# Kernel tuning notes

Hardware: AMD Instinct MI355X
Metric: run time of the kernel (lower is better)

## Reference

```python
import jax, jax.numpy as jnp
import numpy as np
from jax import lax

B, C, D, H, W = 4, 384, 16, 16, 16
DSTATE, DCONV, EXPAND = 16, 4, 2
DIN = C * EXPAND            # 768
DTRANK = (C + 15) // 16     # 24
EPS = 1e-5


def setup_inputs() -> dict:
    ks = jax.random.split(jax.random.key(0), 12)
    g = lambda k, shape, s=0.02: jax.random.normal(k, shape, jnp.float32) * s
    return {
        "x": jax.random.normal(ks[0], (B, C, D, H, W), jnp.float32),
        "gsc_w1": g(ks[1], (C, C, 3, 3, 3)), "gsc_b1": jnp.zeros((C,), jnp.float32),
        "gsc_w2": g(ks[2], (C, C, 3, 3, 3)), "gsc_b2": jnp.zeros((C,), jnp.float32),
        "gsc_w3": g(ks[3], (C, C, 1, 1, 1)), "gsc_b3": jnp.zeros((C,), jnp.float32),
        "gsc_w4": g(ks[4], (C, C, 1, 1, 1)), "gsc_b4": jnp.zeros((C,), jnp.float32),
        "ln_g": jnp.ones((C,), jnp.float32), "ln_b": jnp.zeros((C,), jnp.float32),
        "in_proj_w": g(ks[5], (2 * DIN, C)),
        "conv1d_w": g(ks[6], (DIN, 1, DCONV), 0.1), "conv1d_b": jnp.zeros((DIN,), jnp.float32),
        "x_proj_w": g(ks[7], (DTRANK + 2 * DSTATE, DIN)),
        "dt_proj_w": g(ks[8], (DIN, DTRANK), 0.1), "dt_proj_b": jnp.full((DIN,), -4.0, jnp.float32),
        "A_log": jnp.log(jnp.tile(jnp.arange(1, DSTATE + 1, dtype=jnp.float32), (DIN, 1))),
        "D_skip": jnp.ones((DIN,), jnp.float32),
        "out_proj_w": g(ks[9], (C, DIN)),
    }


def _conv3d(x, w, b, pad):
    y = lax.conv_general_dilated(x, w, (1, 1, 1), [(pad, pad)] * 3,
                                 dimension_numbers=("NCDHW", "OIDHW", "NCDHW"))
    return y + b[None, :, None, None, None]


def _inorm(x):  # InstanceNorm3d, affine=False, biased variance
    m = x.mean((2, 3, 4), keepdims=True)
    v = x.var((2, 3, 4), keepdims=True)
    return (x - m) * lax.rsqrt(v + EPS)


def _forward(x, gsc_w1, gsc_b1, gsc_w2, gsc_b2, gsc_w3, gsc_b3, gsc_w4, gsc_b4,
             ln_g, ln_b, in_proj_w, conv1d_w, conv1d_b, x_proj_w,
             dt_proj_w, dt_proj_b, A_log, D_skip, out_proj_w):
    relu = jax.nn.relu
    # ---- GSC block (residual gated spatial conv) ----
    x1 = relu(_inorm(_conv3d(x, gsc_w1, gsc_b1, 1)))
    x1 = relu(_inorm(_conv3d(x1, gsc_w2, gsc_b2, 1)))
    x2 = relu(_inorm(_conv3d(x, gsc_w3, gsc_b3, 0)))
    xg = relu(_inorm(_conv3d(x1 + x2, gsc_w4, gsc_b4, 0))) + x
    # ---- MambaLayer: flatten voxels to tokens ----
    Bn = xg.shape[0]
    L = D * H * W
    t = xg.reshape(Bn, C, L).swapaxes(1, 2)                     # [B, L, C]
    mu = t.mean(-1, keepdims=True)
    var = t.var(-1, keepdims=True)
    tn = (t - mu) * lax.rsqrt(var + EPS) * ln_g + ln_b          # LayerNorm
    # ---- Mamba block ----
    xz = tn @ in_proj_w.T                                       # [B, L, 2*DIN]
    xin, z = jnp.split(xz, 2, axis=-1)
    xc = xin.swapaxes(1, 2)                                     # [B, DIN, L]
    xc = lax.conv_general_dilated(xc, conv1d_w, (1,), [(DCONV - 1, 0)],
                                  dimension_numbers=("NCH", "OIH", "NCH"),
                                  feature_group_count=DIN)      # causal depthwise conv
    u = jax.nn.silu(xc + conv1d_b[None, :, None]).swapaxes(1, 2)  # [B, L, DIN]
    dbl = u @ x_proj_w.T                                        # [B, L, DTRANK+2N]
    dt, Bm, Cm = jnp.split(dbl, [DTRANK, DTRANK + DSTATE], axis=-1)
    dt = jax.nn.softplus(dt @ dt_proj_w.T + dt_proj_b)          # [B, L, DIN]
    A = -jnp.exp(A_log)                                         # [DIN, N]

    def step(h, inp):  # h: [B, DIN, N]
        dt_t, B_t, C_t, u_t = inp
        dA = jnp.exp(dt_t[:, :, None] * A)
        h = dA * h + (dt_t * u_t)[:, :, None] * B_t[:, None, :]
        return h, jnp.einsum("bdn,bn->bd", h, C_t)

    h0 = jnp.zeros((Bn, DIN, DSTATE), x.dtype)
    _, ys = lax.scan(step, h0, (dt.swapaxes(0, 1), Bm.swapaxes(0, 1),
                                Cm.swapaxes(0, 1), u.swapaxes(0, 1)))
    y = ys.swapaxes(0, 1) + u * D_skip                          # [B, L, DIN]
    y = y * jax.nn.silu(z)
    out = y @ out_proj_w.T                                      # [B, L, C]
    return out.swapaxes(1, 2).reshape(Bn, C, D, H, W)


def reference(x, gsc_w1, gsc_b1, gsc_w2, gsc_b2, gsc_w3, gsc_b3, gsc_w4, gsc_b4,
              ln_g, ln_b, in_proj_w, conv1d_w, conv1d_b, x_proj_w,
              dt_proj_w, dt_proj_b, A_log, D_skip, out_proj_w):
    return _forward(x, gsc_w1, gsc_b1, gsc_w2, gsc_b2, gsc_w3, gsc_b3, gsc_w4, gsc_b4,
                    ln_g, ln_b, in_proj_w, conv1d_w, conv1d_b, x_proj_w,
                    dt_proj_w, dt_proj_b, A_log, D_skip, out_proj_w)
```

## Files before the change

### kernel.cpp

```cpp
#include <hip/hip_runtime.h>
#include <math.h>

#define CDIM 384
#define SDIM 4096
#define BDIM 4
#define DINC 768
#define NST  16
#define NCHUNK 64
#define LCHUNK 64
#define PSTRIDE 6291456

typedef unsigned short ushort_t;
typedef unsigned int uint_t;
typedef __attribute__((ext_vector_type(4))) float f32x4;
typedef __attribute__((ext_vector_type(8))) short bf16x8;

__device__ __forceinline__ ushort_t f2bf(float f) {
    union { float f; uint_t u; } v; v.f = f;
    uint_t r = v.u + 0x7FFFu + ((v.u >> 16) & 1u);
    return (ushort_t)(r >> 16);
}
__device__ __forceinline__ float bf2f(ushort_t u) {
    union { uint_t i; float f; } v; v.i = ((uint_t)u) << 16; return v.f;
}
__device__ __forceinline__ uint_t pk2(float a, float b) {
    return (uint_t)f2bf(a) | ((uint_t)f2bf(b) << 16);
}
__device__ __forceinline__ void gl16(const ushort_t* g, ushort_t* l) {
    __builtin_amdgcn_global_load_lds(
        (const __attribute__((address_space(1))) void*)(g),
        (__attribute__((address_space(3))) void*)(l), 16, 0, 0);
}

__device__ __forceinline__ void wconv_body(const float* __restrict__ W,
                                           ushort_t* __restrict__ Wb, int idx) {
    const float* wp = W + (size_t)idx * 27;
#pragma unroll
    for (int tap = 0; tap < 27; ++tap)
        Wb[(size_t)tap * (CDIM * CDIM) + idx] = f2bf(wp[tap]);
}
__device__ __forceinline__ void cvt_body(const float* __restrict__ src,
                                         ushort_t* __restrict__ dst, int i) {
    float4 v = ((const float4*)src)[i];
    uint2 o; o.x = pk2(v.x, v.y); o.y = pk2(v.z, v.w);
    ((uint2*)dst)[i] = o;
}
__global__ __launch_bounds__(256)
void prep_weights_kernel(const float* w1, const float* w2, const float* w3,
                         const float* w4, const float* ipw, const float* opw,
                         const float* xpw,
                         ushort_t* Wb1, ushort_t* Wb2, ushort_t* w3b, ushort_t* w4b,
                         ushort_t* ipwb, ushort_t* opwb, ushort_t* xpwb) {
    const int bid = blockIdx.x, t = threadIdx.x;
    if      (bid < 576)  wconv_body(w1, Wb1, bid * 256 + t);
    else if (bid < 1152) wconv_body(w2, Wb2, (bid - 576) * 256 + t);
    else if (bid < 1296) cvt_body(w3, w3b, (bid - 1152) * 256 + t);
    else if (bid < 1440) cvt_body(w4, w4b, (bid - 1296) * 256 + t);
    else if (bid < 2016) cvt_body(ipw, ipwb, (bid - 1440) * 256 + t);
    else if (bid < 2304) cvt_body(opw, opwb, (bid - 2016) * 256 + t);
    else                 cvt_body(xpw, xpwb, (bid - 2304) * 256 + t);
}

__global__ __launch_bounds__(384)
void pad_kernel(const float* __restrict__ src, ushort_t* __restrict__ Xp) {
    const int blk = blockIdx.x;
    const int b = blk >> 8, d = (blk >> 4) & 15, h = blk & 15;
    const int ci = threadIdx.x;
    const float* sp = src + (size_t)(b * CDIM + ci) * SDIM + d * 256 + h * 16;
    ushort_t* dp = Xp + ((((size_t)(b * 18 + d + 1) * 18) + (h + 1)) * 18 + 1) * CDIM + ci;
#pragma unroll
    for (int w = 0; w < 16; ++w)
        dp[(size_t)w * CDIM] = f2bf(sp[w]);
}

__global__ __launch_bounds__(384)
void pad_fuse2_kernel(const float* __restrict__ P0, const float* __restrict__ P1,
                      const float* __restrict__ stats, ushort_t* __restrict__ Xp) {
    const int blk = blockIdx.x;
    const int b = blk >> 8, d = (blk >> 4) & 15, h = blk & 15;
    const int ci = threadIdx.x;
    const size_t o = (size_t)(b * CDIM + ci) * SDIM + d * 256 + h * 16;
    const float m = stats[(b * CDIM + ci) * 2], r = stats[(b * CDIM + ci) * 2 + 1];
    ushort_t* dp = Xp + ((((size_t)(b * 18 + d + 1) * 18) + (h + 1)) * 18 + 1) * CDIM + ci;
#pragma unroll
    for (int w = 0; w < 16; ++w) {
        const float v = P0[o + w] + P1[o + w];
        dp[(size_t)w * CDIM] = f2bf(fmaxf((v - m) * r, 0.f));
    }
}

__global__ __launch_bounds__(384)
void pad_fuse3_kernel(const float* __restrict__ P0, const float* __restrict__ P1,
                      const float* __restrict__ st2, const float* __restrict__ C3,
                      const float* __restrict__ st3, ushort_t* __restrict__ Xp) {
    const int blk = blockIdx.x;
    const int b = blk >> 8, d = (blk >> 4) & 15, h = blk & 15;
    const int ci = threadIdx.x;
    const size_t o = (size_t)(b * CDIM + ci) * SDIM + d * 256 + h * 16;
    const float m2 = st2[(b * CDIM + ci) * 2], r2 = st2[(b * CDIM + ci) * 2 + 1];
    const float m3 = st3[(b * CDIM + ci) * 2], r3 = st3[(b * CDIM + ci) * 2 + 1];
    ushort_t* dp = Xp + ((((size_t)(b * 18 + d + 1) * 18) + (h + 1)) * 18 + 1) * CDIM + ci;
#pragma unroll
    for (int w = 0; w < 16; ++w) {
        const float x1 = fmaxf((P0[o + w] + P1[o + w] - m2) * r2, 0.f);
        const float x2 = fmaxf((C3[o + w] - m3) * r3, 0.f);
        dp[(size_t)w * CDIM] = f2bf(x1 + x2);
    }
}

template<int MODE>
__global__ __launch_bounds__(256)
void conv_kernel(const ushort_t* __restrict__ Xp, const ushort_t* __restrict__ Wb,
                 const ushort_t* __restrict__ W3, float* __restrict__ Y01,
                 float* __restrict__ Y2) {
    const int wid = blockIdx.x;
    const int ntid = wid & 127;
    const int rest = wid >> 7;
    const int co0 = (rest % 3) * 128;
    const int zz  = rest / 3;
    const int b  = ntid >> 5;
    const int d  = (ntid >> 1) & 15;
    const int h0 = (ntid & 1) * 8;
    const int t = threadIdx.x;
    const int lane = t & 63;
    const int wv = t >> 6;
    const int wy = wv >> 1, wx = wv & 1;

    const bool is1x1 = (MODE == 2) || (MODE == 1 && zz == 2);
    const ushort_t* Wsrc; int tap0, iters, kd0, kh0, kw0; float* Y;
    if (is1x1) {
        Wsrc = W3; tap0 = 0; iters = 12; kd0 = 1; kh0 = 1; kw0 = 1; Y = Y2;
    } else {
        Wsrc = Wb; tap0 = zz ? 14 : 0; iters = (zz ? 13 : 14) * 12;
        kd0 = zz ? 1 : 0; kh0 = zz ? 1 : 0; kw0 = zz ? 2 : 0;
        Y = Y01 + (size_t)zz * PSTRIDE;
    }

    __shared__ __align__(16) ushort_t As[4096];
    __shared__ __align__(16) ushort_t Bs[4096];

    f32x4 acc[4][4];
#pragma unroll
    for (int i = 0; i < 4; ++i)
#pragma unroll
        for (int j = 0; j < 4; ++j) acc[i][j] = (f32x4){0.f, 0.f, 0.f, 0.f};

    const int l4 = lane >> 2;
    const int cg = (((lane & 3) ^ ((lane >> 3) & 3)) << 3);
    int aTC[2], bTC[2];
#pragma unroll
    for (int i = 0; i < 2; ++i) {
        const int r = wv * 32 + i * 16 + l4;
        aTC[i] = (co0 + r) * CDIM + cg;
        bTC[i] = ((r >> 4) * 18 + (r & 15)) * CDIM + cg;
    }
    ushort_t* lA[2] = { &As[wv * 1024], &As[wv * 1024 + 512] };
    ushort_t* lB[2] = { &Bs[wv * 1024], &Bs[wv * 1024 + 512] };

    int aoff = tap0 * (CDIM * CDIM);
    int goff = (((b * 18 + d + kd0) * 18 + (h0 + kh0)) * 18 + kw0) * CDIM;
    int c12 = 0, ckw = kw0, ckh = kh0;

    const int lm = lane & 15;
    const int sw8 = (((lane >> 4) ^ ((lm >> 1) & 3)) << 3);
    const int rA0 = (wy * 64 + lm) * 32 + sw8;
    const int rB0 = (wx * 64 + lm) * 32 + sw8;

    for (int idx = 0; idx < iters; ++idx) {
#pragma unroll
        for (int i = 0; i < 2; ++i) {
            gl16(Wsrc + aoff + aTC[i], lA[i]);
            gl16(Xp + goff + bTC[i], lB[i]);
        }
        aoff += 32; goff += 32;
        if (++c12 == 12) {
            c12 = 0;
            aoff += CDIM * CDIM - CDIM;
            if (++ckw == 3) {
                ckw = 0;
                if (++ckh == 3) { ckh = 0; goff += 109440; }
                else goff += 5760;
            }
        }
        __syncthreads();
        bf16x8 af[4], bfr[4];
#pragma unroll
        for (int mi = 0; mi < 4; ++mi)
            af[mi] = *reinterpret_cast<const bf16x8*>(&As[rA0 + mi * 512]);
#pragma unroll
        for (int ni = 0; ni < 4; ++ni)
            bfr[ni] = *reinterpret_cast<const bf16x8*>(&Bs[rB0 + ni * 512]);
#pragma unroll
        for (int mi = 0; mi < 4; ++mi)
#pragma unroll
            for (int ni = 0; ni < 4; ++ni)
                acc[mi][ni] = __builtin_amdgcn_mfma_f32_16x16x32_bf16(
                    af[mi], bfr[ni], acc[mi][ni], 0, 0, 0);
        __syncthreads();
    }

    const int coB = co0 + wy * 64 + (lane >> 4) * 4;
    const int nB  = wx * 64 + lm;
#pragma unroll
    for (int mi = 0; mi < 4; ++mi) {
#pragma unroll
        for (int ni = 0; ni < 4; ++ni) {
            const int nl = nB + ni * 16;
            const int s = d * 256 + (h0 + (nl >> 4)) * 16 + (nl & 15);
            float* yp = Y + ((size_t)b * CDIM + (coB + mi * 16)) * SDIM + s;
#pragma unroll
            for (int j = 0; j < 4; ++j)
                yp[(size_t)j * SDIM] = acc[mi][ni][j];
        }
    }
}

template<int EPI>
__global__ __launch_bounds__(256)
void gemm_mfma_kernel(const ushort_t* __restrict__ A, const ushort_t* __restrict__ Bw,
                      void* __restrict__ Cv, void* __restrict__ C2v,
                      int M, int N, int K, int ldc, int nx) {
    const int wid = blockIdx.x;
    const int n0 = (wid % nx) * 128;
    const int m0 = (wid / nx) * 128;
    const int t = threadIdx.x;
    const int lane = t & 63;
    const int wy = (t >> 6) >> 1, wx = (t >> 6) & 1;

    __shared__ ushort_t As[2][128 * 40];
    __shared__ ushort_t Bs[2][128 * 40];

    f32x4 acc[4][4];
#pragma unroll
    for (int i = 0; i < 4; ++i)
#pragma unroll
        for (int j = 0; j < 4; ++j) acc[i][j] = (f32x4){0.f, 0.f, 0.f, 0.f};

    const int arow = t >> 1, half = t & 1;
    const int wA = arow * 40 + half * 16;
    const int lm = lane & 15, lk = (lane >> 4) * 8;
    const int rA0 = (wy * 64 + lm) * 40 + lk;
    const int rB0 = (wx * 64 + lm) * 40 + lk;

    uint4 ra0, ra1, rb0, rb1;

    auto loadg = [&](int kk) {
        const int kb = kk * 32 + half * 16;
        const uint4* pa = reinterpret_cast<const uint4*>(
            A + (size_t)(m0 + arow) * K + kb);
        ra0 = pa[0]; ra1 = pa[1];
        if (n0 + arow < N) {
            const uint4* pb = reinterpret_cast<const uint4*>(
                Bw + (size_t)(n0 + arow) * K + kb);
            rb0 = pb[0]; rb1 = pb[1];
        } else {
            rb0 = make_uint4(0, 0, 0, 0); rb1 = rb0;
        }
    };
    auto lwrite = [&](int buf) {
        *reinterpret_cast<uint4*>(&As[buf][wA])     = ra0;
        *reinterpret_cast<uint4*>(&As[buf][wA + 8]) = ra1;
        *reinterpret_cast<uint4*>(&Bs[buf][wA])     = rb0;
        *reinterpret_cast<uint4*>(&Bs[buf][wA + 8]) = rb1;
    };

    const int KI = K >> 5;
    loadg(0);
    lwrite(0);
    __syncthreads();

    int buf = 0;
    for (int kk = 0; kk < KI; ++kk) {
        const bool more = (kk + 1) < KI;
        if (more) loadg(kk + 1);
        bf16x8 af[4], bfr[4];
#pragma unroll
        for (int mi = 0; mi < 4; ++mi)
            af[mi] = *reinterpret_cast<const bf16x8*>(&As[buf][rA0 + mi * 640]);
#pragma unroll
        for (int ni = 0; ni < 4; ++ni)
            bfr[ni] = *reinterpret_cast<const bf16x8*>(&Bs[buf][rB0 + ni * 640]);
#pragma unroll
        for (int mi = 0; mi < 4; ++mi)
#pragma unroll
            for (int ni = 0; ni < 4; ++ni)
                acc[mi][ni] = __builtin_amdgcn_mfma_f32_16x16x32_bf16(
                    af[mi], bfr[ni], acc[mi][ni], 0, 0, 0);
        if (more) lwrite(buf ^ 1);
        __syncthreads();
        buf ^= 1;
    }

    const int mB = m0 + wy * 64 + (lane >> 4) * 4;
    const int nB = n0 + wx * 64 + lm;
#pragma unroll
    for (int mi = 0; mi < 4; ++mi) {
#pragma unroll
        for (int ni = 0; ni < 4; ++ni) {
            const int n = nB + ni * 16;
            if (EPI == 2) {
                const int mrow = mB + mi * 16;
                const int bb = mrow >> 12, l = mrow & 4095;
                float4 st = {acc[mi][ni][0], acc[mi][ni][1],
                             acc[mi][ni][2], acc[mi][ni][3]};
                *reinterpret_cast<float4*>(
                    (float*)Cv + ((size_t)(bb * CDIM + n)) * SDIM + l) = st;
            } else {
#pragma unroll
                for (int j = 0; j < 4; ++j) {
                    const int m = mB + mi * 16 + j;
                    const float v = acc[mi][ni][j];
                    if (EPI == 0) {
                        if (n < N) ((float*)Cv)[(size_t)m * ldc + n] = v;
                    } else {
                        if (n < DINC) ((ushort_t*)Cv)[(size_t)m * DINC + n] = f2bf(v);
                        else ((ushort_t*)C2v)[(size_t)m * DINC + (n - DINC)] = f2bf(v);
                    }
                }
            }
        }
    }
}

__device__ __forceinline__ void stats_reduce(float s, float ss, float* out) {
#pragma unroll
    for (int off = 32; off > 0; off >>= 1) {
        s += __shfl_down(s, off);
        ss += __shfl_down(ss, off);
    }
    __shared__ float rs[4], rss[4];
    const int wid = threadIdx.x >> 6;
    if ((threadIdx.x & 63) == 0) { rs[wid] = s; rss[wid] = ss; }
    __syncthreads();
    if (threadIdx.x == 0) {
        float S = rs[0] + rs[1] + rs[2] + rs[3];
        float SS = rss[0] + rss[1] + rss[2] + rss[3];
        float m = S * (1.f / SDIM);
        float var = SS * (1.f / SDIM) - m * m;
        out[0] = m;
        out[1] = rsqrtf(var + 1e-5f);
    }
}

__global__ __launch_bounds__(256)
void inorm_stats_combo_kernel(const float* __restrict__ P0, const float* __restrict__ P1,
                              float* __restrict__ SA, const float* __restrict__ X3,
                              float* __restrict__ SB) {
    const int bid = blockIdx.x;
    float s = 0.f, ss = 0.f;
    if (bid < 1536) {
        const float* p0 = P0 + (size_t)bid * SDIM;
        const float* p1 = P1 + (size_t)bid * SDIM;
        for (int i = threadIdx.x * 4; i < SDIM; i += 1024) {
            float4 a = *(const float4*)(p0 + i);
            float4 c = *(const float4*)(p1 + i);
            const float vx = a.x + c.x, vy = a.y + c.y, vz = a.z + c.z, vw = a.w + c.w;
            s += vx + vy + vz + vw;
            ss += vx * vx + vy * vy + vz * vz + vw * vw;
        }
        stats_reduce(s, ss, SA + bid * 2);
    } else {
        const int bc = bid - 1536;
        const float* xp = X3 + (size_t)bc * SDIM;
        for (int i = threadIdx.x * 4; i < SDIM; i += 1024) {
            float4 v = *(const float4*)(xp + i);
            s += v.x + v.y + v.z + v.w;
            ss += v.x * v.x + v.y * v.y + v.z * v.z + v.w * v.w;
        }
        stats_reduce(s, ss, SB + bc * 2);
    }
}

__global__ __launch_bounds__(256)
void inorm_stats_kernel(const float* __restrict__ X, float* __restrict__ stats) {
    const int bc = blockIdx.x;
    const float* xp = X + (size_t)bc * SDIM;
    float s = 0.f, ss = 0.f;
    for (int i = threadIdx.x * 4; i < SDIM; i += 1024) {
        float4 v = *(const float4*)(xp + i);
        s += v.x + v.y + v.z + v.w;
        ss += v.x * v.x + v.y * v.y + v.z * v.z + v.w * v.w;
    }
    stats_reduce(s, ss, stats + bc * 2);
}

__global__ __launch_bounds__(256)
void layernorm_kernel(const float* __restrict__ C4, const float* __restrict__ stats,
                      const float* __restrict__ X, const float* __restrict__ gam,
                      const float* __restrict__ bet, ushort_t* __restrict__ Tn) {
    const int token = blockIdx.x * 4 + (threadIdx.x >> 6);
    const int lane = threadIdx.x & 63;
    const int b = token >> 12, l = token & 4095;
    const size_t base = (size_t)b * CDIM * SDIM + l;
    float v[6];
    float s = 0.f, ss = 0.f;
#pragma unroll
    for (int i = 0; i < 6; ++i) {
        const int c = lane + i * 64;
        const size_t o = base + (size_t)c * SDIM;
        const float m = stats[(b * CDIM + c) * 2], r = stats[(b * CDIM + c) * 2 + 1];
        v[i] = fmaxf((C4[o] - m) * r, 0.f) + X[o];
        s += v[i]; ss += v[i] * v[i];
    }
#pragma unroll
    for (int off = 32; off > 0; off >>= 1) {
        s += __shfl_down(s, off);
        ss += __shfl_down(ss, off);
    }
    s = __shfl(s, 0); ss = __shfl(ss, 0);
    const float m = s * (1.f / CDIM);
    const float r = rsqrtf(ss * (1.f / CDIM) - m * m + 1e-5f);
    ushort_t* tp = Tn + (size_t)token * CDIM;
#pragma unroll
    for (int i = 0; i < 6; ++i) {
        const int c = lane + i * 64;
        tp[c] = f2bf((v[i] - m) * r * gam[c] + bet[c]);
    }
}

__global__ __launch_bounds__(256)
void gemm_dtproj_kernel(const float* __restrict__ A, const float* __restrict__ B,
                        ushort_t* __restrict__ C, const float* __restrict__ bias,
                        int M, int N, int K, int lda, int ldb, int ldc) {
    __shared__ __align__(16) float As[16][132];
    __shared__ __align__(16) float Bs[16][68];
    const int t = threadIdx.x;
    const int m0 = blockIdx.y * 128;
    const int n0 = blockIdx.x * 64;

    float acc[8][4];
#pragma unroll
    for (int i = 0; i < 8; ++i)
#pragma unroll
        for (int j = 0; j < 4; ++j) acc[i][j] = 0.f;

    const int mr = (t & 15) * 8;
    const int nr = (t >> 4) * 4;

    for (int k0 = 0; k0 < K; k0 += 16) {
#pragma unroll
        for (int idx = 0; idx < 8; ++idx) {
            const int e = idx * 256 + t;
            const int k = e & 15, m = e >> 4;
            float v = 0.f;
            if (k0 + k < K) v = A[(size_t)(m0 + m) * lda + (k0 + k)];
            As[k][m] = v;
        }
#pragma unroll
        for (int idx = 0; idx < 4; ++idx) {
            const int e = idx * 256 + t;
            const int k = e & 15, n = e >> 4;
            float v = 0.f;
            if ((n0 + n) < N && (k0 + k) < K) v = B[(size_t)(n0 + n) * ldb + (k0 + k)];
            Bs[k][n] = v;
        }
        __syncthreads();
#pragma unroll
        for (int k = 0; k < 16; ++k) {
            float4 a0 = *(const float4*)&As[k][mr];
            float4 a1 = *(const float4*)&As[k][mr + 4];
            float4 b0 = *(const float4*)&Bs[k][nr];
            const float av[8] = {a0.x, a0.y, a0.z, a0.w, a1.x, a1.y, a1.z, a1.w};
            const float bv[4] = {b0.x, b0.y, b0.z, b0.w};
#pragma unroll
            for (int i = 0; i < 8; ++i)
#pragma unroll
                for (int j = 0; j < 4; ++j)
                    acc[i][j] = fmaf(av[i], bv[j], acc[i][j]);
        }
        __syncthreads();
    }

#pragma unroll
    for (int i = 0; i < 8; ++i) {
        const int m = m0 + mr + i;
#pragma unroll
        for (int j = 0; j < 4; ++j) {
            const int n = n0 + nr + j;
            if (n >= N) continue;
            float v = acc[i][j] + bias[n];
            v = (v > 20.f) ? v : log1pf(__expf(v));
            C[(size_t)m * ldc + n] = f2bf(v);
        }
    }
}

__global__ __launch_bounds__(256)
void dwconv_silu_kernel(const ushort_t* __restrict__ Xin, const float* __restrict__ W,
                        const float* __restrict__ bias, ushort_t* __restrict__ U) {
    const int dch = blockIdx.x * 256 + threadIdx.x;
    const int l0 = blockIdx.y * 4, b = blockIdx.z;
    const float4 w4 = ((const float4*)W)[dch];
    const float wk[4] = {w4.x, w4.y, w4.z, w4.w};
    const float bs = bias[dch];
    const size_t base = ((size_t)b * 4096 + l0) * DINC + dch;
    float r[7];
#pragma unroll
    for (int k = 0; k < 7; ++k) {
        const int ll = l0 - 3 + k;
        r[k] = (ll >= 0) ? bf2f(Xin[base + (size_t)(k - 3) * DINC]) : 0.f;
    }
#pragma unroll
    for (int j = 0; j < 4; ++j) {
        float acc = bs;
#pragma unroll
        for (int k = 0; k < 4; ++k) acc = fmaf(r[j + k], wk[k], acc);
        U[base + (size_t)j * DINC] = f2bf(acc / (1.f + __expf(-acc)));
    }
}

__global__ __launch_bounds__(256)
void scan_phase1_kernel(const ushort_t* __restrict__ DT, const ushort_t* __restrict__ U,
                        const float* __restrict__ DBL, const float* __restrict__ A_log,
                        float* __restrict__ HOUT, float* __restrict__ SDT) {
    const int b = blockIdx.z, chunk = blockIdx.y;
    const int dch = blockIdx.x * 256 + threadIdx.x;
    float Arow[16];
#pragma unroll
    for (int n = 0; n < NST; ++n) Arow[n] = -__expf(A_log[dch * NST + n]);

    __shared__ float bcs[LCHUNK][16];
    const size_t tokbase = (size_t)b * 4096 + chunk * LCHUNK;
#pragma unroll
    for (int idx = 0; idx < 4; ++idx) {
        const int e = idx * 256 + threadIdx.x;
        bcs[e >> 4][e & 15] = DBL[(tokbase + (e >> 4)) * 56 + 24 + (e & 15)];
    }
    __syncthreads();

    size_t off = tokbase * DINC + dch;
    float h[16];
#pragma unroll
    for (int n = 0; n < NST; ++n) h[n] = 0.f;
    float sdt = 0.f;
    float cdt = bf2f(DT[off]), cu = bf2f(U[off]);
    for (int t = 0; t < LCHUNK; ++t) {
        float ndt = 0.f, nu = 0.f;
        if (t < LCHUNK - 1) { ndt = bf2f(DT[off + DINC]); nu = bf2f(U[off + DINC]); }
        sdt += cdt;
        const float du = cdt * cu;
#pragma unroll
        for (int n = 0; n < NST; ++n)
            h[n] = __expf(cdt * Arow[n]) * h[n] + du * bcs[t][n];
        off += DINC;
        cdt = ndt; cu = nu;
    }
    float* hp = HOUT + (((size_t)(b * DINC + dch) * NCHUNK + chunk) << 4);
#pragma unroll
    for (int n = 0; n < NST; ++n) hp[n] = h[n];
    SDT[(size_t)(b * DINC + dch) * NCHUNK + chunk] = sdt;
}

__global__ __launch_bounds__(256)
void scan_phase2_kernel(float* __restrict__ HOUT, const float* __restrict__ SDT,
                        const float* __restrict__ A_log) {
    const int t = blockIdx.x * 256 + threadIdx.x;
    const int b = t / (DINC * NST);
    const int rem = t - b * (DINC * NST);
    const int d = rem >> 4, n = rem & 15;
    const float An = -__expf(A_log[d * NST + n]);
    float* hp = HOUT + (((size_t)(b * DINC + d) * NCHUNK) << 4) + n;
    const float* sp = SDT + (size_t)(b * DINC + d) * NCHUNK;
    float H = 0.f;
    for (int c = 0; c < NCHUNK; ++c) {
        const float tmp = hp[c * 16];
        const float dA = __expf(An * sp[c]);
        hp[c * 16] = H;
        H = dA * H + tmp;
    }
}

__global__ __launch_bounds__(256)
void scan_phase3_kernel(ushort_t* __restrict__ DT, const ushort_t* __restrict__ U,
                        const float* __restrict__ DBL, const ushort_t* __restrict__ Z,
                        const float* __restrict__ A_log, const float* __restrict__ D_skip,
                        const float* __restrict__ HOUT) {
    const int b = blockIdx.z, chunk = blockIdx.y;
    const int dch = blockIdx.x * 256 + threadIdx.x;
    float Arow[16];
#pragma unroll
    for (int n = 0; n < NST; ++n) Arow[n] = -__expf(A_log[dch * NST + n]);
    const float Dsk = D_skip[dch];

    __shared__ float bcs[LCHUNK][32];
    const size_t tokbase = (size_t)b * 4096 + chunk * LCHUNK;
#pragma unroll
    for (int idx = 0; idx < 8; ++idx) {
        const int e = idx * 256 + threadIdx.x;
        bcs[e >> 5][e & 31] = DBL[(tokbase + (e >> 5)) * 56 + 24 + (e & 31)];
    }
    __syncthreads();

    float h[16];
    const float* hp = HOUT + (((size_t)(b * DINC + dch) * NCHUNK + chunk) << 4);
#pragma unroll
    for (int n = 0; n < NST; ++n) h[n] = hp[n];

    size_t off = tokbase * DINC + dch;
    float cdt = bf2f(DT[off]), cu = bf2f(U[off]), cz = bf2f(Z[off]);
    for (int t = 0; t < LCHUNK; ++t) {
        float ndt = 0.f, nu = 0.f, nz = 0.f;
        if (t < LCHUNK - 1) {
            ndt = bf2f(DT[off + DINC]); nu = bf2f(U[off + DINC]); nz = bf2f(Z[off + DINC]);
        }
        const float du = cdt * cu;
        float y = 0.f;
#pragma unroll
        for (int n = 0; n < NST; ++n) {
            h[n] = __expf(cdt * Arow[n]) * h[n] + du * bcs[t][n];
            y = fmaf(h[n], bcs[t][16 + n], y);
        }
        y += cu * Dsk;
        const float sz = cz / (1.f + __expf(-cz));
        DT[off] = f2bf(y * sz);
        off += DINC;
        cdt = ndt; cu = nu; cz = nz;
    }
}

extern "C" void kernel_launch(void* const* d_in, const int* in_sizes, int n_in,
                              void* d_out, int out_size, void* d_ws, size_t ws_size,
                              hipStream_t stream) {
    (void)in_sizes; (void)n_in; (void)out_size; (void)ws_size;
    const float* x         = (const float*)d_in[0];
    const float* w1        = (const float*)d_in[1];
    const float* w2        = (const float*)d_in[3];
    const float* w3        = (const float*)d_in[5];
    const float* w4        = (const float*)d_in[7];
    const float* ln_g      = (const float*)d_in[9];
    const float* ln_b      = (const float*)d_in[10];
    const float* in_proj_w = (const float*)d_in[11];
    const float* conv1d_w  = (const float*)d_in[12];
    const float* conv1d_b  = (const float*)d_in[13];
    const float* x_proj_w  = (const float*)d_in[14];
    const float* dt_proj_w = (const float*)d_in[15];
    const float* dt_proj_b = (const float*)d_in[16];
    const float* A_log     = (const float*)d_in[17];
    const float* D_skip    = (const float*)d_in[18];
    const float* out_proj_w= (const float*)d_in[19];
    float* out = (float*)d_out;

    float* ws = (float*)d_ws;
    float* R0 = ws;
    float* R1 = ws + 6291456;
    float* R2 = ws + 12582912;
    float* R3 = ws + 25165824;
    float* R4 = ws + 37748736;

    float*    P0    = R0;
    float*    P1    = R1;
    ushort_t* Wb1   = (ushort_t*)R2;
    ushort_t* Xp    = (ushort_t*)(R2 + 2097152);
    ushort_t* w3b   = (ushort_t*)(R2 + 6576128);
    ushort_t* w4b   = (ushort_t*)(R2 + 6649856);
    ushort_t* Wb2   = (ushort_t*)(R2 + 6723584);
    float*    SA    = R4;
    float*    SB    = R4 + 4096;
    ushort_t* ipwb  = (ushort_t*)(R4 + 6291456);
    ushort_t* opwb  = (ushort_t*)(R4 + 6586368);
    ushort_t* xpwb  = (ushort_t*)(R4 + 6733824);
    ushort_t* tnb   = (ushort_t*)R0;
    float*    DBL   = R0 + 3145728;
    float*    HOUT  = R1;
    float*    SDT   = R1 + 3145728;
    ushort_t* XIN   = (ushort_t*)R2;
    ushort_t* Zb    = (ushort_t*)R3;
    ushort_t* Ub    = (ushort_t*)R4;
    ushort_t* DTb   = (ushort_t*)R2;

    const size_t XP_BYTES = (size_t)4 * 18 * 18 * 18 * CDIM * 2;

    hipMemsetAsync(Xp, 0, XP_BYTES, stream);
    prep_weights_kernel<<<2346, 256, 0, stream>>>(
        w1, w2, w3, w4, in_proj_w, out_proj_w, x_proj_w,
        Wb1, Wb2, w3b, w4b, ipwb, opwb, xpwb);
    pad_kernel<<<1024, 384, 0, stream>>>(x, Xp);
    conv_kernel<1><<<1152, 256, 0, stream>>>(Xp, Wb1, w3b, P0, R3);
    inorm_stats_combo_kernel<<<3072, 256, 0, stream>>>(P0, P1, SA, R3, SB);
    pad_fuse2_kernel<<<1024, 384, 0, stream>>>(P0, P1, SA, Xp);
    conv_kernel<0><<<768, 256, 0, stream>>>(Xp, Wb2, nullptr, P0, nullptr);
    inorm_stats_combo_kernel<<<1536, 256, 0, stream>>>(P0, P1, SA, nullptr, nullptr);
    pad_fuse3_kernel<<<1024, 384, 0, stream>>>(P0, P1, SA, R3, SB, Xp);
    conv_kernel<2><<<384, 256, 0, stream>>>(Xp, nullptr, w4b, nullptr, R3);
    inorm_stats_kernel<<<1536, 256, 0, stream>>>(R3, SA);
    layernorm_kernel<<<4096, 256, 0, stream>>>(R3, SA, x, ln_g, ln_b, tnb);
    gemm_mfma_kernel<1><<<1536, 256, 0, stream>>>(
        tnb, ipwb, XIN, Zb, 16384, 1536, CDIM, 0, 12);
    dwconv_silu_kernel<<<dim3(3, 1024, 4), 256, 0, stream>>>(XIN, conv1d_w, conv1d_b, Ub);
    gemm_mfma_kernel<0><<<128, 256, 0, stream>>>(
        Ub, xpwb, DBL, nullptr, 16384, 56, DINC, 56, 1);
    gemm_dtproj_kernel<<<dim3(12, 128), 256, 0, stream>>>(
        DBL, dt_proj_w, DTb, dt_proj_b, 16384, DINC, 24, 56, 24, DINC);
    scan_phase1_kernel<<<dim3(3, NCHUNK, 4), 256, 0, stream>>>(
        DTb, Ub, DBL, A_log, HOUT, SDT);
    scan_phase2_kernel<<<192, 256, 0, stream>>>(HOUT, SDT, A_log);
    scan_phase3_kernel<<<dim3(3, NCHUNK, 4), 256, 0, stream>>>(
        DTb, Ub, DBL, Zb, A_log, D_skip, HOUT);
    gemm_mfma_kernel<2><<<384, 256, 0, stream>>>(
        DTb, opwb, out, nullptr, 16384, CDIM, DINC, 0, 3);
}
```

Baseline: 810.2 us.

## Store conv intermediates in bf16, use direct-to-LDS GEMM loads, tile layernorm

Conv outputs (partials P0/P1 and the 1x1 conv results) are now written as bf16 instead of fp32. The instance-norm stats, pad-fuse and layernorm kernels read them with vectorized 16-byte loads, which roughly halves the intermediate memory traffic. The projection GEMMs switch to a gl16 global-to-LDS loading scheme with swizzled shared layout. Layernorm now processes 32 tokens per block through a shared-memory tile so its bf16 output is written coalesced. The cost is extra bf16 rounding of pre-norm activations, which may hurt accuracy, and the GEMM loses its register double buffering.

```diff
diff --git a/kernel.cpp b/kernel.cpp
--- a/kernel.cpp
+++ b/kernel.cpp
@@ -74,24 +74,27 @@
 }
 
 __global__ __launch_bounds__(384)
-void pad_fuse2_kernel(const float* __restrict__ P0, const float* __restrict__ P1,
+void pad_fuse2_kernel(const ushort_t* __restrict__ P0, const ushort_t* __restrict__ P1,
                       const float* __restrict__ stats, ushort_t* __restrict__ Xp) {
     const int blk = blockIdx.x;
     const int b = blk >> 8, d = (blk >> 4) & 15, h = blk & 15;
     const int ci = threadIdx.x;
     const size_t o = (size_t)(b * CDIM + ci) * SDIM + d * 256 + h * 16;
     const float m = stats[(b * CDIM + ci) * 2], r = stats[(b * CDIM + ci) * 2 + 1];
+    union { uint4 q[2]; ushort_t u[16]; } a, c;
+    a.q[0] = ((const uint4*)(P0 + o))[0]; a.q[1] = ((const uint4*)(P0 + o))[1];
+    c.q[0] = ((const uint4*)(P1 + o))[0]; c.q[1] = ((const uint4*)(P1 + o))[1];
     ushort_t* dp = Xp + ((((size_t)(b * 18 + d + 1) * 18) + (h + 1)) * 18 + 1) * CDIM + ci;
 #pragma unroll
     for (int w = 0; w < 16; ++w) {
-        const float v = P0[o + w] + P1[o + w];
+        const float v = bf2f(a.u[w]) + bf2f(c.u[w]);
         dp[(size_t)w * CDIM] = f2bf(fmaxf((v - m) * r, 0.f));
     }
 }
 
 __global__ __launch_bounds__(384)
-void pad_fuse3_kernel(const float* __restrict__ P0, const float* __restrict__ P1,
-                      const float* __restrict__ st2, const float* __restrict__ C3,
+void pad_fuse3_kernel(const ushort_t* __restrict__ P0, const ushort_t* __restrict__ P1,
+                      const float* __restrict__ st2, const ushort_t* __restrict__ C3,
                       const float* __restrict__ st3, ushort_t* __restrict__ Xp) {
     const int blk = blockIdx.x;
     const int b = blk >> 8, d = (blk >> 4) & 15, h = blk & 15;
@@ -99,11 +102,15 @@
     const size_t o = (size_t)(b * CDIM + ci) * SDIM + d * 256 + h * 16;
     const float m2 = st2[(b * CDIM + ci) * 2], r2 = st2[(b * CDIM + ci) * 2 + 1];
     const float m3 = st3[(b * CDIM + ci) * 2], r3 = st3[(b * CDIM + ci) * 2 + 1];
+    union { uint4 q[2]; ushort_t u[16]; } a, c, e;
+    a.q[0] = ((const uint4*)(P0 + o))[0]; a.q[1] = ((const uint4*)(P0 + o))[1];
+    c.q[0] = ((const uint4*)(P1 + o))[0]; c.q[1] = ((const uint4*)(P1 + o))[1];
+    e.q[0] = ((const uint4*)(C3 + o))[0]; e.q[1] = ((const uint4*)(C3 + o))[1];
     ushort_t* dp = Xp + ((((size_t)(b * 18 + d + 1) * 18) + (h + 1)) * 18 + 1) * CDIM + ci;
 #pragma unroll
     for (int w = 0; w < 16; ++w) {
-        const float x1 = fmaxf((P0[o + w] + P1[o + w] - m2) * r2, 0.f);
-        const float x2 = fmaxf((C3[o + w] - m3) * r3, 0.f);
+        const float x1 = fmaxf((bf2f(a.u[w]) + bf2f(c.u[w]) - m2) * r2, 0.f);
+        const float x2 = fmaxf((bf2f(e.u[w]) - m3) * r3, 0.f);
         dp[(size_t)w * CDIM] = f2bf(x1 + x2);
     }
 }
@@ -111,8 +118,8 @@
 template<int MODE>
 __global__ __launch_bounds__(256)
 void conv_kernel(const ushort_t* __restrict__ Xp, const ushort_t* __restrict__ Wb,
-                 const ushort_t* __restrict__ W3, float* __restrict__ Y01,
-                 float* __restrict__ Y2) {
+                 const ushort_t* __restrict__ W3, ushort_t* __restrict__ Y01,
+                 ushort_t* __restrict__ Y2) {
     const int wid = blockIdx.x;
     const int ntid = wid & 127;
     const int rest = wid >> 7;
@@ -127,7 +134,7 @@
     const int wy = wv >> 1, wx = wv & 1;
 
     const bool is1x1 = (MODE == 2) || (MODE == 1 && zz == 2);
-    const ushort_t* Wsrc; int tap0, iters, kd0, kh0, kw0; float* Y;
+    const ushort_t* Wsrc; int tap0, iters, kd0, kh0, kw0; ushort_t* Y;
     if (is1x1) {
         Wsrc = W3; tap0 = 0; iters = 12; kd0 = 1; kh0 = 1; kw0 = 1; Y = Y2;
     } else {
@@ -207,28 +214,29 @@
         for (int ni = 0; ni < 4; ++ni) {
             const int nl = nB + ni * 16;
             const int s = d * 256 + (h0 + (nl >> 4)) * 16 + (nl & 15);
-            float* yp = Y + ((size_t)b * CDIM + (coB + mi * 16)) * SDIM + s;
+            ushort_t* yp = Y + ((size_t)b * CDIM + (coB + mi * 16)) * SDIM + s;
 #pragma unroll
             for (int j = 0; j < 4; ++j)
-                yp[(size_t)j * SDIM] = acc[mi][ni][j];
+                yp[(size_t)j * SDIM] = f2bf(acc[mi][ni][j]);
         }
     }
 }
 
 template<int EPI>
 __global__ __launch_bounds__(256)
-void gemm_mfma_kernel(const ushort_t* __restrict__ A, const ushort_t* __restrict__ Bw,
-                      void* __restrict__ Cv, void* __restrict__ C2v,
-                      int M, int N, int K, int ldc, int nx) {
+void gemm_gl_kernel(const ushort_t* __restrict__ A, const ushort_t* __restrict__ Bw,
+                    void* __restrict__ Cv, void* __restrict__ C2v,
+                    int M, int N, int K, int ldc, int nx) {
     const int wid = blockIdx.x;
     const int n0 = (wid % nx) * 128;
     const int m0 = (wid / nx) * 128;
     const int t = threadIdx.x;
     const int lane = t & 63;
-    const int wy = (t >> 6) >> 1, wx = (t >> 6) & 1;
-
-    __shared__ ushort_t As[2][128 * 40];
-    __shared__ ushort_t Bs[2][128 * 40];
+    const int wv = t >> 6;
+    const int wy = wv >> 1, wx = wv & 1;
+
+    __shared__ __align__(16) ushort_t As[4096];
+    __shared__ __align__(16) ushort_t Bs[4096];
 
     f32x4 acc[4][4];
 #pragma unroll
@@ -236,59 +244,47 @@
 #pragma unroll
         for (int j = 0; j < 4; ++j) acc[i][j] = (f32x4){0.f, 0.f, 0.f, 0.f};
 
-    const int arow = t >> 1, half = t & 1;
-    const int wA = arow * 40 + half * 16;
-    const int lm = lane & 15, lk = (lane >> 4) * 8;
-    const int rA0 = (wy * 64 + lm) * 40 + lk;
-    const int rB0 = (wx * 64 + lm) * 40 + lk;
-
-    uint4 ra0, ra1, rb0, rb1;
-
-    auto loadg = [&](int kk) {
-        const int kb = kk * 32 + half * 16;
-        const uint4* pa = reinterpret_cast<const uint4*>(
-            A + (size_t)(m0 + arow) * K + kb);
-        ra0 = pa[0]; ra1 = pa[1];
-        if (n0 + arow < N) {
-            const uint4* pb = reinterpret_cast<const uint4*>(
-                Bw + (size_t)(n0 + arow) * K + kb);
-            rb0 = pb[0]; rb1 = pb[1];
-        } else {
-            rb0 = make_uint4(0, 0, 0, 0); rb1 = rb0;
-        }
-    };
-    auto lwrite = [&](int buf) {
-        *reinterpret_cast<uint4*>(&As[buf][wA])     = ra0;
-        *reinterpret_cast<uint4*>(&As[buf][wA + 8]) = ra1;
-        *reinterpret_cast<uint4*>(&Bs[buf][wA])     = rb0;
-        *reinterpret_cast<uint4*>(&Bs[buf][wA + 8]) = rb1;
-    };
+    const int l4 = lane >> 2;
+    const int cg = (((lane & 3) ^ ((lane >> 3) & 3)) << 3);
+    size_t aTC[2], bTC[2];
+#pragma unroll
+    for (int i = 0; i < 2; ++i) {
+        const int r = wv * 32 + i * 16 + l4;
+        aTC[i] = (size_t)(m0 + r) * K + cg;
+        int br = n0 + r; if (br >= N) br = N - 1;
+        bTC[i] = (size_t)br * K + cg;
+    }
+    ushort_t* lA[2] = { &As[wv * 1024], &As[wv * 1024 + 512] };
+    ushort_t* lB[2] = { &Bs[wv * 1024], &Bs[wv * 1024 + 512] };
+
+    const int lm = lane & 15;
+    const int sw8 = (((lane >> 4) ^ ((lm >> 1) & 3)) << 3);
+    const int rA0 = (wy * 64 + lm) * 32 + sw8;
+    const int rB0 = (wx * 64 + lm) * 32 + sw8;
 
     const int KI = K >> 5;
-    loadg(0);
-    lwrite(0);
-    __syncthreads();
-
-    int buf = 0;
     for (int kk = 0; kk < KI; ++kk) {
-        const bool more = (kk + 1) < KI;
-        if (more) loadg(kk + 1);
+        const int ko = kk * 32;
+#pragma unroll
+        for (int i = 0; i < 2; ++i) {
+            gl16(A + aTC[i] + ko, lA[i]);
+            gl16(Bw + bTC[i] + ko, lB[i]);
+        }
+        __syncthreads();
         bf16x8 af[4], bfr[4];
 #pragma unroll
         for (int mi = 0; mi < 4; ++mi)
-            af[mi] = *reinterpret_cast<const bf16x8*>(&As[buf][rA0 + mi * 640]);
+            af[mi] = *reinterpret_cast<const bf16x8*>(&As[rA0 + mi * 512]);
 #pragma unroll
         for (int ni = 0; ni < 4; ++ni)
-            bfr[ni] = *reinterpret_cast<const bf16x8*>(&Bs[buf][rB0 + ni * 640]);
+            bfr[ni] = *reinterpret_cast<const bf16x8*>(&Bs[rB0 + ni * 512]);
 #pragma unroll
         for (int mi = 0; mi < 4; ++mi)
 #pragma unroll
             for (int ni = 0; ni < 4; ++ni)
                 acc[mi][ni] = __builtin_amdgcn_mfma_f32_16x16x32_bf16(
                     af[mi], bfr[ni], acc[mi][ni], 0, 0, 0);
-        if (more) lwrite(buf ^ 1);
         __syncthreads();
-        buf ^= 1;
     }
 
     const int mB = m0 + wy * 64 + (lane >> 4) * 4;
@@ -343,79 +339,123 @@
 }
 
 __global__ __launch_bounds__(256)
-void inorm_stats_combo_kernel(const float* __restrict__ P0, const float* __restrict__ P1,
-                              float* __restrict__ SA, const float* __restrict__ X3,
+void inorm_stats_combo_kernel(const ushort_t* __restrict__ P0,
+                              const ushort_t* __restrict__ P1,
+                              float* __restrict__ SA,
+                              const ushort_t* __restrict__ X3,
                               float* __restrict__ SB) {
     const int bid = blockIdx.x;
     float s = 0.f, ss = 0.f;
     if (bid < 1536) {
-        const float* p0 = P0 + (size_t)bid * SDIM;
-        const float* p1 = P1 + (size_t)bid * SDIM;
-        for (int i = threadIdx.x * 4; i < SDIM; i += 1024) {
-            float4 a = *(const float4*)(p0 + i);
-            float4 c = *(const float4*)(p1 + i);
-            const float vx = a.x + c.x, vy = a.y + c.y, vz = a.z + c.z, vw = a.w + c.w;
-            s += vx + vy + vz + vw;
-            ss += vx * vx + vy * vy + vz * vz + vw * vw;
+        const ushort_t* p0 = P0 + (size_t)bid * SDIM;
+        const ushort_t* p1 = P1 + (size_t)bid * SDIM;
+        for (int i = threadIdx.x * 8; i < SDIM; i += 2048) {
+            union { uint4 q; ushort_t u[8]; } a, c;
+            a.q = *(const uint4*)(p0 + i);
+            c.q = *(const uint4*)(p1 + i);
+#pragma unroll
+            for (int j = 0; j < 8; ++j) {
+                const float v = bf2f(a.u[j]) + bf2f(c.u[j]);
+                s += v; ss += v * v;
+            }
         }
         stats_reduce(s, ss, SA + bid * 2);
     } else {
         const int bc = bid - 1536;
-        const float* xp = X3 + (size_t)bc * SDIM;
-        for (int i = threadIdx.x * 4; i < SDIM; i += 1024) {
-            float4 v = *(const float4*)(xp + i);
-            s += v.x + v.y + v.z + v.w;
-            ss += v.x * v.x + v.y * v.y + v.z * v.z + v.w * v.w;
+        const ushort_t* xp = X3 + (size_t)bc * SDIM;
+        for (int i = threadIdx.x * 8; i < SDIM; i += 2048) {
+            union { uint4 q; ushort_t u[8]; } a;
+            a.q = *(const uint4*)(xp + i);
+#pragma unroll
+            for (int j = 0; j < 8; ++j) {
+                const float v = bf2f(a.u[j]);
+                s += v; ss += v * v;
+            }
         }
         stats_reduce(s, ss, SB + bc * 2);
     }
 }
 
 __global__ __launch_bounds__(256)
-void inorm_stats_kernel(const float* __restrict__ X, float* __restrict__ stats) {
+void inorm_stats_kernel(const ushort_t* __restrict__ X, float* __restrict__ stats) {
     const int bc = blockIdx.x;
-    const float* xp = X + (size_t)bc * SDIM;
+    const ushort_t* xp = X + (size_t)bc * SDIM;
     float s = 0.f, ss = 0.f;
-    for (int i = threadIdx.x * 4; i < SDIM; i += 1024) {
-        float4 v = *(const float4*)(xp + i);
-        s += v.x + v.y + v.z + v.w;
-        ss += v.x * v.x + v.y * v.y + v.z * v.z + v.w * v.w;
+    for (int i = threadIdx.x * 8; i < SDIM; i += 2048) {
+        union { uint4 q; ushort_t u[8]; } a;
+        a.q = *(const uint4*)(xp + i);
+#pragma unroll
+        for (int j = 0; j < 8; ++j) {
+            const float v = bf2f(a.u[j]);
+            s += v; ss += v * v;
+        }
     }
     stats_reduce(s, ss, stats + bc * 2);
 }
 
 __global__ __launch_bounds__(256)
-void layernorm_kernel(const float* __restrict__ C4, const float* __restrict__ stats,
+void layernorm_kernel(const ushort_t* __restrict__ C4, const float* __restrict__ stats,
                       const float* __restrict__ X, const float* __restrict__ gam,
                       const float* __restrict__ bet, ushort_t* __restrict__ Tn) {
-    const int token = blockIdx.x * 4 + (threadIdx.x >> 6);
+    const int blk = blockIdx.x;
+    const int b = blk >> 7;
+    const int tile0 = (blk & 127) * 32;
+    const int wv = threadIdx.x >> 6;
     const int lane = threadIdx.x & 63;
-    const int b = token >> 12, l = token & 4095;
-    const size_t base = (size_t)b * CDIM * SDIM + l;
-    float v[6];
-    float s = 0.f, ss = 0.f;
+    const int l0 = tile0 + wv * 8;
+
+    __shared__ ushort_t tile[32 * 384];
+
+    float v[6][8];
+    float s[8], ss[8];
+#pragma unroll
+    for (int t = 0; t < 8; ++t) { s[t] = 0.f; ss[t] = 0.f; }
+    float g[6], be[6];
+
 #pragma unroll
     for (int i = 0; i < 6; ++i) {
         const int c = lane + i * 64;
-        const size_t o = base + (size_t)c * SDIM;
-        const float m = stats[(b * CDIM + c) * 2], r = stats[(b * CDIM + c) * 2 + 1];
-        v[i] = fmaxf((C4[o] - m) * r, 0.f) + X[o];
-        s += v[i]; ss += v[i] * v[i];
+        g[i] = gam[c]; be[i] = bet[c];
+        const size_t base = (size_t)(b * CDIM + c) * SDIM + l0;
+        union { uint4 q; ushort_t u[8]; } cv;
+        cv.q = *(const uint4*)(C4 + base);
+        const float4 x0 = *(const float4*)(X + base);
+        const float4 x1 = *(const float4*)(X + base + 4);
+        const float xs[8] = {x0.x, x0.y, x0.z, x0.w, x1.x, x1.y, x1.z, x1.w};
+        const float m = stats[(b * CDIM + c) * 2];
+        const float r = stats[(b * CDIM + c) * 2 + 1];
+#pragma unroll
+        for (int t = 0; t < 8; ++t) {
+            const float val = fmaxf((bf2f(cv.u[t]) - m) * r, 0.f) + xs[t];
+            v[i][t] = val;
+            s[t] += val; ss[t] += val * val;
+        }
     }
 #pragma unroll
     for (int off = 32; off > 0; off >>= 1) {
-        s += __shfl_down(s, off);
-        ss += __shfl_down(ss, off);
-    }
-    s = __shfl(s, 0); ss = __shfl(ss, 0);
-    const float m = s * (1.f / CDIM);
-    const float r = rsqrtf(ss * (1.f / CDIM) - m * m + 1e-5f);
-    ushort_t* tp = Tn + (size_t)token * CDIM;
-#pragma unroll
-    for (int i = 0; i < 6; ++i) {
-        const int c = lane + i * 64;
-        tp[c] = f2bf((v[i] - m) * r * gam[c] + bet[c]);
-    }
+#pragma unroll
+        for (int t = 0; t < 8; ++t) {
+            s[t] += __shfl_xor(s[t], off);
+            ss[t] += __shfl_xor(ss[t], off);
+        }
+    }
+#pragma unroll
+    for (int t = 0; t < 8; ++t) {
+        const float mean = s[t] * (1.f / CDIM);
+        const float rstd = rsqrtf(ss[t] * (1.f / CDIM) - mean * mean + 1e-5f);
+        const int trow = (wv * 8 + t) * 384;
+#pragma unroll
+        for (int i = 0; i < 6; ++i) {
+            const int c = lane + i * 64;
+            tile[trow + c] = f2bf((v[i][t] - mean) * rstd * g[i] + be[i]);
+        }
+    }
+    __syncthreads();
+    uint4* dst = (uint4*)(Tn + ((size_t)b * 4096 + tile0) * CDIM);
+    const uint4* srcp = (const uint4*)tile;
+#pragma unroll
+    for (int k = 0; k < 6; ++k)
+        dst[k * 256 + threadIdx.x] = srcp[k * 256 + threadIdx.x];
 }
 
 __global__ __launch_bounds__(256)
@@ -647,8 +687,9 @@
     float* R3 = ws + 25165824;
     float* R4 = ws + 37748736;
 
-    float*    P0    = R0;
-    float*    P1    = R1;
+    ushort_t* P0    = (ushort_t*)R0;
+    ushort_t* P1    = P0 + PSTRIDE;
+    ushort_t* C34   = (ushort_t*)R3;
     ushort_t* Wb1   = (ushort_t*)R2;
     ushort_t* Xp    = (ushort_t*)(R2 + 2097152);
     ushort_t* w3b   = (ushort_t*)(R2 + 6576128);
@@ -675,19 +716,19 @@
         w1, w2, w3, w4, in_proj_w, out_proj_w, x_proj_w,
         Wb1, Wb2, w3b, w4b, ipwb, opwb, xpwb);
     pad_kernel<<<1024, 384, 0, stream>>>(x, Xp);
-    conv_kernel<1><<<1152, 256, 0, stream>>>(Xp, Wb1, w3b, P0, R3);
-    inorm_stats_combo_kernel<<<3072, 256, 0, stream>>>(P0, P1, SA, R3, SB);
+    conv_kernel<1><<<1152, 256, 0, stream>>>(Xp, Wb1, w3b, P0, C34);
+    inorm_stats_combo_kernel<<<3072, 256, 0, stream>>>(P0, P1, SA, C34, SB);
     pad_fuse2_kernel<<<1024, 384, 0, stream>>>(P0, P1, SA, Xp);
     conv_kernel<0><<<768, 256, 0, stream>>>(Xp, Wb2, nullptr, P0, nullptr);
     inorm_stats_combo_kernel<<<1536, 256, 0, stream>>>(P0, P1, SA, nullptr, nullptr);
-    pad_fuse3_kernel<<<1024, 384, 0, stream>>>(P0, P1, SA, R3, SB, Xp);
-    conv_kernel<2><<<384, 256, 0, stream>>>(Xp, nullptr, w4b, nullptr, R3);
-    inorm_stats_kernel<<<1536, 256, 0, stream>>>(R3, SA);
-    layernorm_kernel<<<4096, 256, 0, stream>>>(R3, SA, x, ln_g, ln_b, tnb);
-    gemm_mfma_kernel<1><<<1536, 256, 0, stream>>>(
+    pad_fuse3_kernel<<<1024, 384, 0, stream>>>(P0, P1, SA, C34, SB, Xp);
+    conv_kernel<2><<<384, 256, 0, stream>>>(Xp, nullptr, w4b, nullptr, C34);
+    inorm_stats_kernel<<<1536, 256, 0, stream>>>(C34, SA);
+    layernorm_kernel<<<512, 256, 0, stream>>>(C34, SA, x, ln_g, ln_b, tnb);
+    gemm_gl_kernel<1><<<1536, 256, 0, stream>>>(
         tnb, ipwb, XIN, Zb, 16384, 1536, CDIM, 0, 12);
     dwconv_silu_kernel<<<dim3(3, 1024, 4), 256, 0, stream>>>(XIN, conv1d_w, conv1d_b, Ub);
-    gemm_mfma_kernel<0><<<128, 256, 0, stream>>>(
+    gemm_gl_kernel<0><<<128, 256, 0, stream>>>(
         Ub, xpwb, DBL, nullptr, 16384, 56, DINC, 56, 1);
     gemm_dtproj_kernel<<<dim3(12, 128), 256, 0, stream>>>(
         DBL, dt_proj_w, DTb, dt_proj_b, 16384, DINC, 24, 56, 24, DINC);
@@ -696,6 +737,6 @@
     scan_phase2_kernel<<<192, 256, 0, stream>>>(HOUT, SDT, A_log);
     scan_phase3_kernel<<<dim3(3, NCHUNK, 4), 256, 0, stream>>>(
         DTb, Ub, DBL, Zb, A_log, D_skip, HOUT);
-    gemm_mfma_kernel<2><<<384, 256, 0, stream>>>(
+    gemm_gl_kernel<2><<<384, 256, 0, stream>>>(
         DTb, opwb, out, nullptr, 16384, CDIM, DINC, 0, 3);
 }
```

Result: faster. 750.8 us (-7.3%).
